# Kernel tuning notes

Measured on AMD Instinct MI355X. Metric: run time of the kernel, lower is better.

Reference implementation:

```python
import jax, jax.numpy as jnp
import numpy as np

B, S, D_IN = 4, 2048, 2048
H, HD, G = 16, 128, 4
D_OUT = H * HD  # 2048
EPS = 1e-6
NEG_INF = -1e9


def zc_rmsnorm(x, scale):
    # zero-centered RMSNorm, computed in fp32
    xf = x.astype(jnp.float32)
    rms = jax.lax.rsqrt(jnp.mean(xf * xf, axis=-1, keepdims=True) + EPS)
    return (xf * rms * (1.0 + scale)).astype(x.dtype)


def rope(x, cos, sin):
    # x: (b, h, s, d); cos/sin: (s, d) -> broadcast over (b, h)
    d = x.shape[-1]
    x1, x2 = x[..., : d // 2], x[..., d // 2 :]
    rotated = jnp.concatenate([-x2, x1], axis=-1)
    return x * cos[None, None] + rotated * sin[None, None]


def setup_inputs() -> dict:
    key = jax.random.key(0)
    ks = jax.random.split(key, 8)
    x = jax.random.normal(ks[0], (B, S, D_IN), dtype=jnp.float32)
    # causal mask: True = masked out (upper triangle above diagonal)
    mask = jnp.triu(jnp.ones((S, S), dtype=bool), k=1)
    attn_mask = jnp.ones((B, S), dtype=bool)  # True = valid token
    # RoPE tables
    pos = jnp.arange(S, dtype=jnp.float32)
    inv = 1.0 / (10000.0 ** (jnp.arange(0, HD, 2, dtype=jnp.float32) / HD))
    ang = pos[:, None] * inv[None, :]              # (S, HD/2)
    ang = jnp.concatenate([ang, ang], axis=-1)     # (S, HD)
    cos, sin = jnp.cos(ang), jnp.sin(ang)
    s_in = 1.0 / np.sqrt(D_IN)
    Wq = jax.random.normal(ks[1], (D_IN, D_OUT), dtype=jnp.float32) * s_in
    Wk = jax.random.normal(ks[2], (D_IN, G * HD), dtype=jnp.float32) * s_in
    Wv = jax.random.normal(ks[3], (D_IN, G * HD), dtype=jnp.float32) * s_in
    Wg = jax.random.normal(ks[4], (D_IN, D_OUT), dtype=jnp.float32) * s_in
    Wo = jax.random.normal(ks[5], (D_OUT, D_IN), dtype=jnp.float32) / np.sqrt(D_OUT)
    q_scale = jnp.zeros((HD,), dtype=jnp.float32)
    k_scale = jnp.zeros((HD,), dtype=jnp.float32)
    return {"x": x, "mask": mask, "attn_mask": attn_mask, "cos": cos, "sin": sin,
            "Wq": Wq, "Wk": Wk, "Wv": Wv, "Wg": Wg, "Wo": Wo,
            "q_scale": q_scale, "k_scale": k_scale}


def reference(x, mask, attn_mask, cos, sin, Wq, Wk, Wv, Wg, Wo, q_scale, k_scale):
    b, s, _ = x.shape
    q = (x @ Wq).reshape(b, s, H, HD).transpose(0, 2, 1, 3)   # (b,H,s,hd)
    k = (x @ Wk).reshape(b, s, G, HD).transpose(0, 2, 1, 3)   # (b,G,s,hd)
    v = (x @ Wv).reshape(b, s, G, HD).transpose(0, 2, 1, 3)   # (b,G,s,hd)
    gate = jax.nn.sigmoid(x @ Wg)                             # (b,s,d_out)

    q = zc_rmsnorm(q, q_scale)
    k = zc_rmsnorm(k, k_scale)
    q = rope(q, cos[:s], sin[:s])
    k = rope(k, cos[:s], sin[:s])

    # GQA: repeat kv heads
    rep = H // G
    k = jnp.repeat(k, rep, axis=1)   # (b,H,s,hd)
    v = jnp.repeat(v, rep, axis=1)

    # combined mask: True = masked out
    curr = mask[:s, :s][None, None] | (~attn_mask[:, None, None, :s])  # (b,1,s,s)
    scores = jnp.einsum("bhqd,bhkd->bhqk", q, k) / np.sqrt(HD)
    scores = jnp.where(curr, NEG_INF, scores)
    attn = jax.nn.softmax(scores, axis=-1)
    ctx = jnp.einsum("bhqk,bhkd->bhqd", attn, v)              # (b,H,s,hd)
    ctx = ctx.transpose(0, 2, 1, 3).reshape(b, s, D_OUT)
    ctx = ctx * gate
    return ctx @ Wo
```

## Files before the change

kernel.cpp:

```cpp
#include <hip/hip_runtime.h>

typedef _Float16 half_t;
typedef _Float16 f16x8 __attribute__((ext_vector_type(8)));
typedef float    f32x4 __attribute__((ext_vector_type(4)));

typedef __attribute__((address_space(1))) const void void_g;
typedef __attribute__((address_space(3))) void void_l;
#define GLOAD_LDS16(gp, lp) __builtin_amdgcn_global_load_lds((void_g*)(gp), (void_l*)(lp), 16, 0, 0)

constexpr int B_ = 4, S_ = 2048, DIN_ = 2048, H_ = 16, HD_ = 128, G_ = 4, DOUT_ = 2048;
constexpr int NC_ = 5120;

__global__ __launch_bounds__(256) void cvt_f16(const float* __restrict__ in,
                                               half_t* __restrict__ out, int n4) {
  int i = blockIdx.x * blockDim.x + threadIdx.x;
  if (i < n4) {
    float4 v = reinterpret_cast<const float4*>(in)[i];
    union { half_t h[4]; uint2 u; } pk;
    pk.h[0] = (half_t)v.x; pk.h[1] = (half_t)v.y;
    pk.h[2] = (half_t)v.z; pk.h[3] = (half_t)v.w;
    reinterpret_cast<uint2*>(out)[i] = pk.u;
  }
}

__global__ __launch_bounds__(256) void transpose_cvt(const float* __restrict__ in,
                                                     half_t* __restrict__ out, int R, int C) {
  __shared__ float t[32][33];
  int tx = threadIdx.x, ty = threadIdx.y;
  int c0 = blockIdx.x * 32, r0 = blockIdx.y * 32;
#pragma unroll
  for (int i = ty; i < 32; i += 8) t[i][tx] = in[(size_t)(r0 + i) * C + c0 + tx];
  __syncthreads();
#pragma unroll
  for (int i = ty; i < 32; i += 8)
    out[(size_t)(c0 + i) * R + r0 + tx] = (half_t)t[tx][i];
}

__device__ __forceinline__ void storeC(half_t* p, float v) { *p = (half_t)v; }
__device__ __forceinline__ void storeC(float* p, float v)  { *p = v; }

#define BARRIER   asm volatile("s_barrier" ::: "memory")
#define LGKM0     asm volatile("s_waitcnt lgkmcnt(0)" ::: "memory"); __builtin_amdgcn_sched_barrier(0)
#define VMCNT3    asm volatile("s_waitcnt vmcnt(3)" ::: "memory")

template <typename OutT>
__global__ __launch_bounds__(512, 4) void gemm_bk32(const half_t* __restrict__ A,
                                                    const half_t* __restrict__ Bt,
                                                    OutT* __restrict__ C,
                                                    int M, int N, int K) {
  __shared__ alignas(16) half_t Ash[3][256 * 32];
  __shared__ alignas(16) half_t Bsh[3][128 * 32];
  const int tid  = threadIdx.x;
  const int lane = tid & 63;
  const int wid  = tid >> 6;
  const int lq = lane & 15, lg = lane >> 4;
  const int wm = wid >> 1, wn = wid & 1;

  const int gx = gridDim.x;
  int wgid = blockIdx.y * gx + blockIdx.x;
  const int chunk = (gx * gridDim.y) >> 3;
  wgid = (wgid & 7) * chunk + (wgid >> 3);
  const int mb = wgid / gx, nb = wgid - mb * gx;

  const int nk = K >> 5;

  const int arow0 = wid * 32 + (lane >> 2);
  const int arow1 = arow0 + 16;
  const int brow  = wid * 16 + (lane >> 2);
  const half_t* aSrc0 = A  + (size_t)(mb * 256 + arow0) * K + (((lane & 3) ^ (arow0 & 3)) << 3);
  const half_t* aSrc1 = A  + (size_t)(mb * 256 + arow1) * K + (((lane & 3) ^ (arow1 & 3)) << 3);
  const half_t* bSrc  = Bt + (size_t)(nb * 128 + brow)  * K + (((lane & 3) ^ (brow  & 3)) << 3);

  auto stage = [&](int kt, int bsel) {
    GLOAD_LDS16(aSrc0 + kt * 32, &Ash[bsel][wid * 1024]);
    GLOAD_LDS16(aSrc1 + kt * 32, &Ash[bsel][wid * 1024 + 512]);
    GLOAD_LDS16(bSrc  + kt * 32, &Bsh[bsel][wid * 512]);
  };

  f32x4 acc[4][4];
#pragma unroll
  for (int i = 0; i < 4; ++i)
#pragma unroll
    for (int j = 0; j < 4; ++j) acc[i][j] = (f32x4){0.f, 0.f, 0.f, 0.f};

  const int rdslot = (lg ^ (lq & 3)) * 8;

  stage(0, 0);
  stage(1, 1);
  VMCNT3;
  BARRIER;

  int cur = 0;
#pragma unroll 1
  for (int t = 0; t < nk; ++t) {
    {
      const int kt2 = (t + 2 < nk) ? t + 2 : nk - 1;
      int b2 = cur + 2; if (b2 >= 3) b2 -= 3;
      stage(kt2, b2);
    }
    f16x8 a4[4], b4[4];
#pragma unroll
    for (int mi = 0; mi < 4; ++mi)
      a4[mi] = *reinterpret_cast<const f16x8*>(&Ash[cur][(wm * 64 + mi * 16 + lq) * 32 + rdslot]);
#pragma unroll
    for (int nj = 0; nj < 4; ++nj)
      b4[nj] = *reinterpret_cast<const f16x8*>(&Bsh[cur][(wn * 64 + nj * 16 + lq) * 32 + rdslot]);
    LGKM0;
    __builtin_amdgcn_s_setprio(1);
#pragma unroll
    for (int mi = 0; mi < 4; ++mi)
#pragma unroll
      for (int nj = 0; nj < 4; ++nj)
        acc[mi][nj] = __builtin_amdgcn_mfma_f32_16x16x32_f16(a4[mi], b4[nj], acc[mi][nj], 0, 0, 0);
    __builtin_amdgcn_s_setprio(0);
    VMCNT3;
    BARRIER;
    cur = (cur == 2) ? 0 : cur + 1;
  }

#pragma unroll
  for (int mi = 0; mi < 4; ++mi) {
#pragma unroll
    for (int r = 0; r < 4; ++r) {
      const size_t row = (size_t)(mb * 256 + wm * 64 + mi * 16 + lg * 4 + r);
#pragma unroll
      for (int nj = 0; nj < 4; ++nj) {
        const int col = nb * 128 + wn * 64 + nj * 16 + lq;
        storeC(&C[row * N + col], acc[mi][nj][r]);
      }
    }
  }
}

__global__ __launch_bounds__(256) void post_qk(const half_t* __restrict__ QKVG,
                                               half_t* __restrict__ Q, half_t* __restrict__ Kd,
                                               const float* __restrict__ cosT,
                                               const float* __restrict__ sinT,
                                               const float* __restrict__ q_scale,
                                               const float* __restrict__ k_scale) {
  const int row  = blockIdx.x;
  const int slot = blockIdx.y * 4 + (threadIdx.x >> 6);
  const int lane = threadIdx.x & 63;
  const int b = row >> 11, s = row & (S_ - 1);
  const bool isq = slot < 16;
  const int col0 = isq ? slot * 128 : 2048 + (slot - 16) * 128;
  float x0 = (float)QKVG[(size_t)row * NC_ + col0 + lane];
  float x1 = (float)QKVG[(size_t)row * NC_ + col0 + lane + 64];
  float ss = x0 * x0 + x1 * x1;
#pragma unroll
  for (int m = 1; m < 64; m <<= 1) ss += __shfl_xor(ss, m);
  float rms = rsqrtf(ss * (1.f / 128.f) + 1e-6f);
  const float* sc = isq ? q_scale : k_scale;
  float y0 = x0 * rms * (1.f + sc[lane]);
  float y1 = x1 * rms * (1.f + sc[lane + 64]);
  float c0 = cosT[s * 128 + lane], c1 = cosT[s * 128 + lane + 64];
  float s0 = sinT[s * 128 + lane], s1 = sinT[s * 128 + lane + 64];
  float r0 = y0 * c0 - y1 * s0;
  float r1 = y1 * c1 + y0 * s1;
  if (isq) { r0 *= 0.12751743f; r1 *= 0.12751743f; }
  half_t* dst = isq ? (Q  + ((size_t)(b * H_ + slot) * S_ + s) * HD_)
                    : (Kd + ((size_t)(b * G_ + slot - 16) * S_ + s) * HD_);
  dst[lane]      = (half_t)r0;
  dst[lane + 64] = (half_t)r1;
}

__global__ __launch_bounds__(256) void v_transpose(const half_t* __restrict__ QKVG,
                                                   half_t* __restrict__ VT) {
  __shared__ half_t t[32][33];
  int tx = threadIdx.x, ty = threadIdx.y;
  int s0 = blockIdx.x * 32, d0 = blockIdx.y * 32;
  int bg = blockIdx.z;
  int b = bg >> 2, g = bg & 3;
#pragma unroll
  for (int i = ty; i < 32; i += 8)
    t[i][tx] = QKVG[(size_t)(b * S_ + s0 + i) * NC_ + 2560 + g * 128 + d0 + tx];
  __syncthreads();
#pragma unroll
  for (int i = ty; i < 32; i += 8)
    VT[((size_t)bg * 128 + d0 + i) * S_ + s0 + tx] = t[tx][i];
}

__global__ __launch_bounds__(256) void flash_attn4(const half_t* __restrict__ Q,
                                                   const half_t* __restrict__ K,
                                                   const half_t* __restrict__ VT,
                                                   const half_t* __restrict__ QKVG,
                                                   half_t* __restrict__ ctxg) {
  __shared__ alignas(16) half_t Klds[3][32 * 128];
  __shared__ alignas(16) half_t Vlds[3][128 * 32];
  __shared__ alignas(16) half_t Plds[4][2][16 * 40];

  const int lane = threadIdx.x & 63;
  const int wid  = threadIdx.x >> 6;
  const int lq = lane & 15, lg = lane >> 4;
  const int qa = blockIdx.x;
  const int h = blockIdx.y, b = blockIdx.z;
  const int g = h >> 2;

  const half_t* Kb = K  + ((size_t)(b * G_ + g) * S_) * HD_;
  const half_t* Vb = VT + ((size_t)(b * G_ + g) * HD_) * S_;

  auto stage = [&](int kb, int bsel) {
#pragma unroll
    for (int ii = 0; ii < 2; ++ii) {
      const int i = wid * 2 + ii;
      {
        const int row  = i * 4 + lg;
        const int csrc = (lq * 16) ^ ((row & 7) << 4);
        GLOAD_LDS16(Kb + (size_t)(kb + row) * HD_ + (csrc >> 1), &Klds[bsel][i * 512]);
      }
      {
        const int d    = i * 16 + (lane >> 2);
        const int csrc = ((lane & 3) * 16) ^ (((d >> 1) & 3) << 4);
        GLOAD_LDS16(Vb + (size_t)d * S_ + kb + (csrc >> 1), &Vlds[bsel][i * 512]);
      }
    }
  };

#pragma unroll 1
  for (int seg = 0; seg < 2; ++seg) {
    const int qt = seg ? (15 - qa) : qa;
    const int q0w = qt * 128 + wid * 32;
    const half_t* Qb = Q + ((size_t)(b * H_ + h) * S_ + q0w) * HD_;

    f16x8 qf[2][4];
#pragma unroll
    for (int qs = 0; qs < 2; ++qs)
#pragma unroll
      for (int kc = 0; kc < 4; ++kc)
        qf[qs][kc] = *reinterpret_cast<const f16x8*>(Qb + (size_t)(qs * 16 + lq) * HD_ + kc * 32 + lg * 8);

    f32x4 O[2][8];
#pragma unroll
    for (int qs = 0; qs < 2; ++qs)
#pragma unroll
      for (int nc = 0; nc < 8; ++nc) O[qs][nc] = (f32x4){0.f, 0.f, 0.f, 0.f};
    float lf[2] = {0.f, 0.f};

    const int nt = 4 * qt + 4;
    const int qmax = q0w + 31;

    if (seg) {
      asm volatile("s_waitcnt vmcnt(0)" ::: "memory");
      __builtin_amdgcn_s_barrier();
    }
    stage(0, 0);
    stage(32, 1);
    asm volatile("s_waitcnt vmcnt(4)" ::: "memory");
    __builtin_amdgcn_s_barrier();

    int cur = 0;
#pragma unroll 1
    for (int t = 0; t < nt; ++t) {
      {
        const int t2 = (t + 2 < nt) ? t + 2 : nt - 1;
        int b2 = cur + 2; if (b2 >= 3) b2 -= 3;
        stage(t2 * 32, b2);
      }
      const int kb = t * 32;
      if (kb <= qmax) {
        const half_t* kbuf = Klds[cur];
        const half_t* vbuf = Vlds[cur];
        f32x4 sA[2][2];
#pragma unroll
        for (int qs = 0; qs < 2; ++qs)
#pragma unroll
          for (int ks = 0; ks < 2; ++ks) sA[qs][ks] = (f32x4){0.f, 0.f, 0.f, 0.f};
        __builtin_amdgcn_s_setprio(1);
#pragma unroll
        for (int kc = 0; kc < 4; ++kc)
#pragma unroll
          for (int ks = 0; ks < 2; ++ks) {
            const int row = ks * 16 + lq;
            const int off = row * 128 + ((((kc * 64 + lg * 16)) ^ ((row & 7) << 4)) >> 1);
            f16x8 kf = *reinterpret_cast<const f16x8*>(kbuf + off);
            sA[0][ks] = __builtin_amdgcn_mfma_f32_16x16x32_f16(kf, qf[0][kc], sA[0][ks], 0, 0, 0);
            sA[1][ks] = __builtin_amdgcn_mfma_f32_16x16x32_f16(kf, qf[1][kc], sA[1][ks], 0, 0, 0);
          }
        __builtin_amdgcn_s_setprio(0);
        f16x8 pf[2];
#pragma unroll
        for (int qs = 0; qs < 2; ++qs) {
          const int qg = q0w + qs * 16 + lq;
          const bool diag = (kb + 31 > q0w + qs * 16);
          float rs = 0.f;
          union { half_t hh[8]; uint2 u2[2]; } pk;
#pragma unroll
          for (int ks = 0; ks < 2; ++ks)
#pragma unroll
            for (int r = 0; r < 4; ++r) {
              float sv = sA[qs][ks][r];
              if (diag) {
                const int key = kb + ks * 16 + lg * 4 + r;
                if (key > qg) sv = -1e9f;
              }
              const float p = __builtin_amdgcn_exp2f(sv - 1.5f);
              rs += p;
              pk.hh[ks * 4 + r] = (half_t)p;
            }
          lf[qs] += rs;
          half_t* Pw = &Plds[wid][qs][0];
          *reinterpret_cast<uint2*>(Pw + lq * 40 + lg * 4)      = pk.u2[0];
          *reinterpret_cast<uint2*>(Pw + lq * 40 + 16 + lg * 4) = pk.u2[1];
        }
        pf[0] = *reinterpret_cast<const f16x8*>(&Plds[wid][0][0] + lq * 40 + lg * 8);
        pf[1] = *reinterpret_cast<const f16x8*>(&Plds[wid][1][0] + lq * 40 + lg * 8);
        __builtin_amdgcn_s_setprio(1);
#pragma unroll
        for (int nc = 0; nc < 8; ++nc) {
          const int d = nc * 16 + lq;
          const int off = d * 32 + (((lg * 16) ^ (((d >> 1) & 3) << 4)) >> 1);
          f16x8 vf = *reinterpret_cast<const f16x8*>(vbuf + off);
          O[0][nc] = __builtin_amdgcn_mfma_f32_16x16x32_f16(vf, pf[0], O[0][nc], 0, 0, 0);
          O[1][nc] = __builtin_amdgcn_mfma_f32_16x16x32_f16(vf, pf[1], O[1][nc], 0, 0, 0);
        }
        __builtin_amdgcn_s_setprio(0);
      }
      asm volatile("s_waitcnt vmcnt(4)" ::: "memory");
      __builtin_amdgcn_s_barrier();
      cur = (cur == 2) ? 0 : cur + 1;
    }

#pragma unroll
    for (int qs = 0; qs < 2; ++qs) {
      float l = lf[qs];
      l += __shfl_xor(l, 16);
      l += __shfl_xor(l, 32);
      const float linv = 1.f / l;
      const int qg = q0w + qs * 16 + lq;
      const size_t row = (size_t)b * S_ + qg;
#pragma unroll
      for (int nc = 0; nc < 8; ++nc) {
        const int col = h * 128 + nc * 16 + lg * 4;
        union { uint2 u; half_t hh[4]; } gg;
        gg.u = *reinterpret_cast<const uint2*>(QKVG + row * NC_ + 3072 + col);
        union { half_t hh[4]; uint2 u; } ov;
#pragma unroll
        for (int r = 0; r < 4; ++r) {
          const float gate = 1.f / (1.f + __expf(-(float)gg.hh[r]));
          ov.hh[r] = (half_t)(O[qs][nc][r] * linv * gate);
        }
        *reinterpret_cast<uint2*>(ctxg + row * DOUT_ + col) = ov.u;
      }
    }
  }
}

extern "C" void kernel_launch(void* const* d_in, const int* in_sizes, int n_in,
                              void* d_out, int out_size, void* d_ws, size_t ws_size,
                              hipStream_t stream) {
  const float* x     = (const float*)d_in[0];
  const float* cosT  = (const float*)d_in[3];
  const float* sinT  = (const float*)d_in[4];
  const float* Wq    = (const float*)d_in[5];
  const float* Wk    = (const float*)d_in[6];
  const float* Wv    = (const float*)d_in[7];
  const float* Wg    = (const float*)d_in[8];
  const float* Wo    = (const float*)d_in[9];
  const float* q_scale = (const float*)d_in[10];
  const float* k_scale = (const float*)d_in[11];
  float* out = (float*)d_out;

  const size_t MB = 1ull << 20;
  char* w = (char*)d_ws;
  half_t* xh   = (half_t*)(w);
  half_t* ctxg = (half_t*)(w);
  half_t* WT   = (half_t*)(w + 32 * MB);
  half_t* WoT  = (half_t*)(w + 52 * MB);
  half_t* QKVG = (half_t*)(w + 60 * MB);
  half_t* Qh   = (half_t*)(w + 140 * MB);
  half_t* Kh   = (half_t*)(w + 172 * MB);
  half_t* VTh  = (half_t*)(w + 180 * MB);

  dim3 tb(32, 8);
  cvt_f16<<<16384, 256, 0, stream>>>(x, xh, B_ * S_ * DIN_ / 4);
  transpose_cvt<<<dim3(64, 64), tb, 0, stream>>>(Wq, WT,                     2048, 2048);
  transpose_cvt<<<dim3(16, 64), tb, 0, stream>>>(Wk, WT + 2048 * 2048,       2048, 512);
  transpose_cvt<<<dim3(16, 64), tb, 0, stream>>>(Wv, WT + 2560 * 2048,       2048, 512);
  transpose_cvt<<<dim3(64, 64), tb, 0, stream>>>(Wg, WT + (size_t)3072 * 2048, 2048, 2048);
  transpose_cvt<<<dim3(64, 64), tb, 0, stream>>>(Wo, WoT,                    2048, 2048);

  gemm_bk32<half_t><<<dim3(40, 32), 512, 0, stream>>>(xh, WT, QKVG, 8192, NC_, 2048);

  post_qk<<<dim3(8192, 5), 256, 0, stream>>>(QKVG, Qh, Kh, cosT, sinT, q_scale, k_scale);
  v_transpose<<<dim3(64, 4, 16), tb, 0, stream>>>(QKVG, VTh);

  flash_attn4<<<dim3(8, 16, 4), 256, 0, stream>>>(Qh, Kh, VTh, QKVG, ctxg);

  gemm_bk32<float><<<dim3(16, 32), 512, 0, stream>>>(ctxg, WoT, out, 8192, 2048, 2048);
}
```

Measured before the change: 490.4 us.

## Enlarge GEMM block tile to 256x256 with 8-wave 2x4 layout

Both projection GEMMs now use a 256x256 output tile per workgroup instead of 256x128. Each wave computes 128x64, which doubles the A fragments held per K step and raises MFMA work per LDS load. The LDS swizzle changes to XOR on (row>>1)&3, and the grid and waitcnt are adjusted to match. The intent is to cut global and LDS traffic per FLOP, at the cost of more registers, lower occupancy (launch bounds 2) and fewer workgroups (640 and 256) to spread across the CUs.

```diff
diff --git a/kernel.cpp b/kernel.cpp
--- a/kernel.cpp
+++ b/kernel.cpp
@@ -41,20 +41,19 @@
 
 #define BARRIER   asm volatile("s_barrier" ::: "memory")
 #define LGKM0     asm volatile("s_waitcnt lgkmcnt(0)" ::: "memory"); __builtin_amdgcn_sched_barrier(0)
-#define VMCNT3    asm volatile("s_waitcnt vmcnt(3)" ::: "memory")
+#define VMCNT4    asm volatile("s_waitcnt vmcnt(4)" ::: "memory")
 
 template <typename OutT>
-__global__ __launch_bounds__(512, 4) void gemm_bk32(const half_t* __restrict__ A,
-                                                    const half_t* __restrict__ Bt,
-                                                    OutT* __restrict__ C,
-                                                    int M, int N, int K) {
+__global__ __launch_bounds__(512, 2) void gemm_big(const half_t* __restrict__ A,
+                                                   const half_t* __restrict__ Bt,
+                                                   OutT* __restrict__ C,
+                                                   int M, int N, int K) {
   __shared__ alignas(16) half_t Ash[3][256 * 32];
-  __shared__ alignas(16) half_t Bsh[3][128 * 32];
-  const int tid  = threadIdx.x;
-  const int lane = tid & 63;
-  const int wid  = tid >> 6;
+  __shared__ alignas(16) half_t Bsh[3][256 * 32];
+  const int lane = threadIdx.x & 63;
+  const int wid  = threadIdx.x >> 6;
   const int lq = lane & 15, lg = lane >> 4;
-  const int wm = wid >> 1, wn = wid & 1;
+  const int wm = wid >> 2, wn = wid & 3;
 
   const int gx = gridDim.x;
   int wgid = blockIdx.y * gx + blockIdx.x;
@@ -64,30 +63,31 @@
 
   const int nk = K >> 5;
 
-  const int arow0 = wid * 32 + (lane >> 2);
-  const int arow1 = arow0 + 16;
-  const int brow  = wid * 16 + (lane >> 2);
-  const half_t* aSrc0 = A  + (size_t)(mb * 256 + arow0) * K + (((lane & 3) ^ (arow0 & 3)) << 3);
-  const half_t* aSrc1 = A  + (size_t)(mb * 256 + arow1) * K + (((lane & 3) ^ (arow1 & 3)) << 3);
-  const half_t* bSrc  = Bt + (size_t)(nb * 128 + brow)  * K + (((lane & 3) ^ (brow  & 3)) << 3);
+  const int r0 = wid * 32 + (lane >> 2);
+  const int r1 = r0 + 16;
+  const half_t* aSrc0 = A  + (size_t)(mb * 256 + r0) * K + (((lane & 3) ^ ((r0 >> 1) & 3)) << 3);
+  const half_t* aSrc1 = A  + (size_t)(mb * 256 + r1) * K + (((lane & 3) ^ ((r1 >> 1) & 3)) << 3);
+  const half_t* bSrc0 = Bt + (size_t)(nb * 256 + r0) * K + (((lane & 3) ^ ((r0 >> 1) & 3)) << 3);
+  const half_t* bSrc1 = Bt + (size_t)(nb * 256 + r1) * K + (((lane & 3) ^ ((r1 >> 1) & 3)) << 3);
 
   auto stage = [&](int kt, int bsel) {
     GLOAD_LDS16(aSrc0 + kt * 32, &Ash[bsel][wid * 1024]);
     GLOAD_LDS16(aSrc1 + kt * 32, &Ash[bsel][wid * 1024 + 512]);
-    GLOAD_LDS16(bSrc  + kt * 32, &Bsh[bsel][wid * 512]);
+    GLOAD_LDS16(bSrc0 + kt * 32, &Bsh[bsel][wid * 1024]);
+    GLOAD_LDS16(bSrc1 + kt * 32, &Bsh[bsel][wid * 1024 + 512]);
   };
 
-  f32x4 acc[4][4];
-#pragma unroll
-  for (int i = 0; i < 4; ++i)
+  f32x4 acc[8][4];
+#pragma unroll
+  for (int i = 0; i < 8; ++i)
 #pragma unroll
     for (int j = 0; j < 4; ++j) acc[i][j] = (f32x4){0.f, 0.f, 0.f, 0.f};
 
-  const int rdslot = (lg ^ (lq & 3)) * 8;
+  const int rdslot = (lg ^ ((lq >> 1) & 3)) * 8;
 
   stage(0, 0);
   stage(1, 1);
-  VMCNT3;
+  VMCNT4;
   BARRIER;
 
   int cur = 0;
@@ -98,34 +98,34 @@
       int b2 = cur + 2; if (b2 >= 3) b2 -= 3;
       stage(kt2, b2);
     }
-    f16x8 a4[4], b4[4];
-#pragma unroll
-    for (int mi = 0; mi < 4; ++mi)
-      a4[mi] = *reinterpret_cast<const f16x8*>(&Ash[cur][(wm * 64 + mi * 16 + lq) * 32 + rdslot]);
+    f16x8 a8[8], b4[4];
+#pragma unroll
+    for (int mi = 0; mi < 8; ++mi)
+      a8[mi] = *reinterpret_cast<const f16x8*>(&Ash[cur][(wm * 128 + mi * 16 + lq) * 32 + rdslot]);
 #pragma unroll
     for (int nj = 0; nj < 4; ++nj)
       b4[nj] = *reinterpret_cast<const f16x8*>(&Bsh[cur][(wn * 64 + nj * 16 + lq) * 32 + rdslot]);
     LGKM0;
     __builtin_amdgcn_s_setprio(1);
 #pragma unroll
-    for (int mi = 0; mi < 4; ++mi)
+    for (int mi = 0; mi < 8; ++mi)
 #pragma unroll
       for (int nj = 0; nj < 4; ++nj)
-        acc[mi][nj] = __builtin_amdgcn_mfma_f32_16x16x32_f16(a4[mi], b4[nj], acc[mi][nj], 0, 0, 0);
+        acc[mi][nj] = __builtin_amdgcn_mfma_f32_16x16x32_f16(a8[mi], b4[nj], acc[mi][nj], 0, 0, 0);
     __builtin_amdgcn_s_setprio(0);
-    VMCNT3;
+    VMCNT4;
     BARRIER;
     cur = (cur == 2) ? 0 : cur + 1;
   }
 
 #pragma unroll
-  for (int mi = 0; mi < 4; ++mi) {
+  for (int mi = 0; mi < 8; ++mi) {
 #pragma unroll
     for (int r = 0; r < 4; ++r) {
-      const size_t row = (size_t)(mb * 256 + wm * 64 + mi * 16 + lg * 4 + r);
+      const size_t row = (size_t)(mb * 256 + wm * 128 + mi * 16 + lg * 4 + r);
 #pragma unroll
       for (int nj = 0; nj < 4; ++nj) {
-        const int col = nb * 128 + wn * 64 + nj * 16 + lq;
+        const int col = nb * 256 + wn * 64 + nj * 16 + lq;
         storeC(&C[row * N + col], acc[mi][nj][r]);
       }
     }
@@ -379,12 +379,12 @@
   transpose_cvt<<<dim3(64, 64), tb, 0, stream>>>(Wg, WT + (size_t)3072 * 2048, 2048, 2048);
   transpose_cvt<<<dim3(64, 64), tb, 0, stream>>>(Wo, WoT,                    2048, 2048);
 
-  gemm_bk32<half_t><<<dim3(40, 32), 512, 0, stream>>>(xh, WT, QKVG, 8192, NC_, 2048);
+  gemm_big<half_t><<<dim3(20, 32), 512, 0, stream>>>(xh, WT, QKVG, 8192, NC_, 2048);
 
   post_qk<<<dim3(8192, 5), 256, 0, stream>>>(QKVG, Qh, Kh, cosT, sinT, q_scale, k_scale);
   v_transpose<<<dim3(64, 4, 16), tb, 0, stream>>>(QKVG, VTh);
 
   flash_attn4<<<dim3(8, 16, 4), 256, 0, stream>>>(Qh, Kh, VTh, QKVG, ctxg);
 
-  gemm_bk32<float><<<dim3(16, 32), 512, 0, stream>>>(ctxg, WoT, out, 8192, 2048, 2048);
-}
+  gemm_big<float><<<dim3(8, 32), 512, 0, stream>>>(ctxg, WoT, out, 8192, 2048, 2048);
+}
```

Measured after the change: 522.4 us. 6.5% more time.
